# Performance work log

Hardware: AMD Instinct MI355X
Metric: run time of the kernel (lower is better)

The kernel has to match this reference:

```python
import jax, jax.numpy as jnp
import numpy as np

BETA = 0.25


def setup_inputs() -> dict:
    key = jax.random.key(0)
    k1, k2 = jax.random.split(key)
    z_e = jax.random.normal(k1, (32, 256, 32, 32), dtype=jnp.float32)
    embedding = jax.random.normal(k2, (1024, 256), dtype=jnp.float32)
    return {"z_e": z_e, "embedding": embedding}


def reference(z_e, embedding):
    B, D, H, W = z_e.shape  # (32, 256, 32, 32)
    K = embedding.shape[0]
    # flatten to (N, D), N = B*H*W
    z_flat = jnp.transpose(z_e, (0, 2, 3, 1)).reshape(-1, D)
    # squared L2 distances: ||z||^2 + ||e||^2 - 2 z.e^T  -> (N, K)
    dist = (
        jnp.sum(z_flat * z_flat, axis=1, keepdims=True)
        + jnp.sum(embedding * embedding, axis=1)
        - 2.0 * z_flat @ embedding.T
    )
    codes = jnp.argmin(dist, axis=1)  # (N,) int
    # gather codebook vectors, reshape back to (B, D, H, W)
    z_q = embedding[codes].reshape(B, H, W, D).transpose(0, 3, 1, 2)
    # commitment loss (mse over all elements)
    sg = jax.lax.stop_gradient
    commit_loss = (
        jnp.mean((sg(z_q) - z_e) ** 2)
        + BETA * jnp.mean((z_q - sg(z_e)) ** 2)
    )
    # straight-through estimator
    z_q_st = z_e + sg(z_q - z_e)
    return z_q_st, codes.reshape(B, H, W), commit_loss
```

## Files before the change

### kernel.cpp

```cpp
#include <hip/hip_runtime.h>

typedef _Float16 f16;
typedef __attribute__((ext_vector_type(4))) _Float16 f16x4;
typedef __attribute__((ext_vector_type(8))) _Float16 f16x8;
typedef __attribute__((ext_vector_type(4))) float f32x4;

#define D_DIM 256
#define K_CB  1024
#define N_TOT 32768
#define DHW   262144
#define ZQ_N  8388608
#define OUT_CODES 8388608
#define OUT_LOSS  8421376

#define WS_BSP   0
#define WS_EN2   262144
#define WS_CODES 263168
#define WS_CNT   295936
#define WS_LIST  296000
#define WS_PART  300096
#define LIST_CAP 4096
#define EPS_GAP  0.01f

__global__ void vq_prep(const float* __restrict__ emb, float* __restrict__ ws) {
    const int k = blockIdx.x;
    const int t = threadIdx.x;
    const float4 v = *reinterpret_cast<const float4*>(emb + k * D_DIM + t * 4);
    float s = v.x * v.x + v.y * v.y + v.z * v.z + v.w * v.w;
#pragma unroll
    for (int off = 32; off > 0; off >>= 1) s += __shfl_down(s, off);
    if (t == 0) ws[WS_EN2 + k] = -0.5f * s;

    const float a[4] = {v.x, v.y, v.z, v.w};
    f16x4 hv, lv;
#pragma unroll
    for (int i = 0; i < 4; ++i) {
        f16 h = (f16)a[i];
        hv[i] = h;
        lv[i] = (f16)(a[i] - (float)h);
    }
    f16* B = reinterpret_cast<f16*>(ws) + k * 512;
    *reinterpret_cast<f16x4*>(B + t * 4)       = hv;
    *reinterpret_cast<f16x4*>(B + 256 + t * 4) = lv;
    if (k == 0 && t == 0) reinterpret_cast<int*>(ws + WS_CNT)[0] = 0;
}

__global__ __launch_bounds__(256, 2) void vq_gemm(const float* __restrict__ z,
                                                  float* ws,
                                                  float* __restrict__ out) {
    __shared__ __align__(16) char lds[81920];
    f16* Ahi = reinterpret_cast<f16*>(lds);
    f16* Alo = reinterpret_cast<f16*>(lds + 32768);
    f16* Bs  = reinterpret_cast<f16*>(lds + 65536);
    float* comb = reinterpret_cast<float*>(lds + 65536);

    const f16* __restrict__ Bsp = reinterpret_cast<const f16*>(ws);
    const float* __restrict__ en2 = ws + WS_EN2;
    const int tid = threadIdx.x;
    const int lane = tid & 63;
    const int w = tid >> 6, wm = w >> 1, wn = w & 1;
    const int r0 = blockIdx.x * 64;
    const float* __restrict__ zb = z + (r0 >> 10) * DHW + (r0 & 1023);

    {
        const int arow = tid & 63;
        const int adg  = tid >> 6;
#pragma unroll
        for (int p = 0; p < 16; ++p) {
            const int d = adg * 64 + p * 4;
            f16x4 hv, lv;
#pragma unroll
            for (int i = 0; i < 4; ++i) {
                const float x = zb[(d + i) * 1024 + arow];
                const f16 h = (f16)x;
                hv[i] = h;
                lv[i] = (f16)(x - (float)h);
            }
            const int byte = (arow * 512 + d * 2) ^ ((arow & 7) << 4);
            *reinterpret_cast<f16x4*>(reinterpret_cast<char*>(Ahi) + byte) = hv;
            *reinterpret_cast<f16x4*>(reinterpret_cast<char*>(Alo) + byte) = lv;
        }
    }

    float bv[8], sv[8];
    int   bk[8];
#pragma unroll
    for (int i = 0; i < 8; ++i) { bv[i] = -3.0e38f; sv[i] = -3.0e38f; bk[i] = 0; }

    f32x4 acc[2][4];
#pragma unroll
    for (int i = 0; i < 2; ++i)
#pragma unroll
        for (int j = 0; j < 4; ++j) acc[i][j] = f32x4{0.f, 0.f, 0.f, 0.f};

    f16x8 breg[4], bnext[4];
    float e2v[4];
#pragma unroll
    for (int p = 0; p < 4; ++p) {
        const int u = tid + p * 256;
        breg[p] = *reinterpret_cast<const f16x8*>(
            Bsp + (u >> 3) * 512 + (u & 7) * 8);
    }

    for (int q = 0; q < 64; ++q) {
        __syncthreads();
#pragma unroll
        for (int p = 0; p < 4; ++p) {
            const int u = tid + p * 256;
            const int col = u >> 3, k8 = (u & 7) * 8;
            const int byte = (col * 128 + k8 * 2) ^ ((col & 7) << 4);
            *reinterpret_cast<f16x8*>(reinterpret_cast<char*>(Bs) + byte) = breg[p];
        }
        if (q < 63) {
            const int qn = q + 1;
            const int c0n = (qn >> 3) << 7;
            const int kbn = (qn & 7) << 6;
#pragma unroll
            for (int p = 0; p < 4; ++p) {
                const int u = tid + p * 256;
                bnext[p] = *reinterpret_cast<const f16x8*>(
                    Bsp + (c0n + (u >> 3)) * 512 + kbn + (u & 7) * 8);
            }
        }
        if ((q & 7) == 6) {
            const int c0 = (q >> 3) << 7;
#pragma unroll
            for (int jf = 0; jf < 4; ++jf)
                e2v[jf] = en2[c0 + wn * 64 + jf * 16 + (lane & 15)];
        }
        __syncthreads();

        const int kA = (q & 3) << 6;
        const bool ehi = ((q >> 2) & 1) == 0;
#pragma unroll
        for (int s = 0; s < 2; ++s) {
            const int kl = s * 32 + (lane >> 4) * 8;
            f16x8 bf[4];
#pragma unroll
            for (int jf = 0; jf < 4; ++jf) {
                const int cc = wn * 64 + jf * 16 + (lane & 15);
                bf[jf] = *reinterpret_cast<const f16x8*>(
                    reinterpret_cast<const char*>(Bs) +
                    ((cc * 128 + kl * 2) ^ ((cc & 7) << 4)));
            }
            f16x8 ah[2];
#pragma unroll
            for (int i = 0; i < 2; ++i) {
                const int row = wm * 32 + i * 16 + (lane & 15);
                ah[i] = *reinterpret_cast<const f16x8*>(
                    reinterpret_cast<const char*>(Ahi) +
                    ((row * 512 + (kA + kl) * 2) ^ ((row & 7) << 4)));
            }
#pragma unroll
            for (int i = 0; i < 2; ++i)
#pragma unroll
                for (int jf = 0; jf < 4; ++jf)
                    acc[i][jf] = __builtin_amdgcn_mfma_f32_16x16x32_f16(
                        ah[i], bf[jf], acc[i][jf], 0, 0, 0);
            if (ehi) {
                f16x8 al[2];
#pragma unroll
                for (int i = 0; i < 2; ++i) {
                    const int row = wm * 32 + i * 16 + (lane & 15);
                    al[i] = *reinterpret_cast<const f16x8*>(
                        reinterpret_cast<const char*>(Alo) +
                        ((row * 512 + (kA + kl) * 2) ^ ((row & 7) << 4)));
                }
#pragma unroll
                for (int i = 0; i < 2; ++i)
#pragma unroll
                    for (int jf = 0; jf < 4; ++jf)
                        acc[i][jf] = __builtin_amdgcn_mfma_f32_16x16x32_f16(
                            al[i], bf[jf], acc[i][jf], 0, 0, 0);
            }
        }

        if ((q & 7) == 7) {
            const int c0 = (q >> 3) << 7;
#pragma unroll
            for (int jf = 0; jf < 4; ++jf) {
                const int col = c0 + wn * 64 + jf * 16 + (lane & 15);
                const float e2 = e2v[jf];
#pragma unroll
                for (int i = 0; i < 2; ++i)
#pragma unroll
                    for (int r = 0; r < 4; ++r) {
                        const float v = acc[i][jf][r] + e2;
                        const int idx = i * 4 + r;
                        if (v > bv[idx]) { sv[idx] = bv[idx]; bv[idx] = v; bk[idx] = col; }
                        else if (v > sv[idx]) sv[idx] = v;
                    }
            }
#pragma unroll
            for (int i = 0; i < 2; ++i)
#pragma unroll
                for (int j = 0; j < 4; ++j) acc[i][j] = f32x4{0.f, 0.f, 0.f, 0.f};
        }
#pragma unroll
        for (int p = 0; p < 4; ++p) breg[p] = bnext[p];
    }

#pragma unroll
    for (int m = 1; m <= 8; m <<= 1)
#pragma unroll
        for (int idx = 0; idx < 8; ++idx) {
            const float pv = __shfl_xor(bv[idx], m);
            const float ps = __shfl_xor(sv[idx], m);
            const int   pk = __shfl_xor(bk[idx], m);
            if (pv > bv[idx] || (pv == bv[idx] && pk < bk[idx])) {
                sv[idx] = fmaxf(bv[idx], ps);
                bv[idx] = pv; bk[idx] = pk;
            } else {
                sv[idx] = fmaxf(sv[idx], pv);
            }
        }

    __syncthreads();
    if ((lane & 15) == 0) {
#pragma unroll
        for (int idx = 0; idx < 8; ++idx) {
            const int row = wm * 32 + (idx >> 2) * 16 + (lane >> 4) * 4 + (idx & 3);
            comb[(wn * 64 + row) * 3 + 0] = bv[idx];
            comb[(wn * 64 + row) * 3 + 1] = sv[idx];
            comb[(wn * 64 + row) * 3 + 2] = __int_as_float(bk[idx]);
        }
    }
    __syncthreads();
    if (tid < 64) {
        const int row = tid;
        const float v0 = comb[row * 3 + 0], s0 = comb[row * 3 + 1];
        const int   k0 = __float_as_int(comb[row * 3 + 2]);
        const float v1 = comb[(64 + row) * 3 + 0], s1 = comb[(64 + row) * 3 + 1];
        const int   k1 = __float_as_int(comb[(64 + row) * 3 + 2]);
        float bvf, svf; int bkf;
        if (v1 > v0 || (v1 == v0 && k1 < k0)) { bvf = v1; bkf = k1; svf = fmaxf(v0, s1); }
        else                                  { bvf = v0; bkf = k0; svf = fmaxf(s0, v1); }
        const int n = r0 + row;
        reinterpret_cast<int*>(ws + WS_CODES)[n] = bkf;
        out[OUT_CODES + n] = (float)bkf;
        if (bvf - svf < EPS_GAP) {
            const int pos = atomicAdd(reinterpret_cast<int*>(ws + WS_CNT), 1);
            if (pos < LIST_CAP) reinterpret_cast<int*>(ws + WS_LIST)[pos] = n;
        }
    }
}

__global__ __launch_bounds__(256) void vq_rescore(const float* __restrict__ z,
                                                  const float* __restrict__ emb,
                                                  float* ws,
                                                  float* __restrict__ out) {
    __shared__ float zl[256];
    __shared__ float rv[4];
    __shared__ int   rk[4];
    const int cnt0 = reinterpret_cast<const int*>(ws + WS_CNT)[0];
    const int cnt = cnt0 < LIST_CAP ? cnt0 : LIST_CAP;
    const int t = threadIdx.x;
    for (int it = blockIdx.x; it < cnt; it += gridDim.x) {
        const int n = reinterpret_cast<const int*>(ws + WS_LIST)[it];
        const int b = n >> 10, hw = n & 1023;
        __syncthreads();
        zl[t] = z[b * DHW + t * 1024 + hw];
        __syncthreads();
        float bvv = -3.0e38f; int bkk = 0;
#pragma unroll
        for (int j = 0; j < 4; ++j) {
            const int k = t + j * 256;
            const float* e = emb + k * D_DIM;
            float dot = 0.f;
#pragma unroll 8
            for (int d = 0; d < 256; d += 4) {
                const float4 ev = *reinterpret_cast<const float4*>(e + d);
                const float4 zv = *reinterpret_cast<const float4*>(zl + d);
                dot += ev.x * zv.x + ev.y * zv.y + ev.z * zv.z + ev.w * zv.w;
            }
            const float v = dot + ws[WS_EN2 + k];
            if (v > bvv || (v == bvv && k < bkk)) { bvv = v; bkk = k; }
        }
#pragma unroll
        for (int m = 1; m <= 32; m <<= 1) {
            const float pv = __shfl_xor(bvv, m);
            const int   pk = __shfl_xor(bkk, m);
            if (pv > bvv || (pv == bvv && pk < bkk)) { bvv = pv; bkk = pk; }
        }
        if ((t & 63) == 0) { rv[t >> 6] = bvv; rk[t >> 6] = bkk; }
        __syncthreads();
        if (t == 0) {
#pragma unroll
            for (int q = 1; q < 4; ++q)
                if (rv[q] > bvv || (rv[q] == bvv && rk[q] < bkk)) { bvv = rv[q]; bkk = rk[q]; }
            reinterpret_cast<int*>(ws + WS_CODES)[n] = bkk;
            out[OUT_CODES + n] = (float)bkk;
        }
    }
}

__global__ __launch_bounds__(256) void vq_gather(const float* __restrict__ z,
                                                 const float* __restrict__ emb,
                                                 float* ws,
                                                 float* __restrict__ out) {
    __shared__ __align__(16) float el[64][260];
    __shared__ int   cl[64];
    __shared__ float red[4];
    const int tid = threadIdx.x;
    const int n0 = blockIdx.x * 64;
    const int b = n0 >> 10, hw0 = n0 & 1023;
    if (tid < 64) cl[tid] = reinterpret_cast<const int*>(ws + WS_CODES)[n0 + tid];
    __syncthreads();
#pragma unroll
    for (int p = 0; p < 16; ++p) {
        const int u = tid + p * 256;
        const int r = u >> 6, f4 = (u & 63) * 4;
        *reinterpret_cast<float4*>(&el[r][f4]) =
            *reinterpret_cast<const float4*>(emb + cl[r] * D_DIM + f4);
    }
    __syncthreads();
    const int hw4 = (tid & 15) * 4, dg = tid >> 4;
    const float* zp = z + b * DHW + hw0 + hw4;
    float* op = out + b * DHW + hw0 + hw4;
    float ls = 0.f;
#pragma unroll
    for (int dd = 0; dd < 16; ++dd) {
        const int d = dg * 16 + dd;
        float4 q;
        q.x = el[hw4 + 0][d]; q.y = el[hw4 + 1][d];
        q.z = el[hw4 + 2][d]; q.w = el[hw4 + 3][d];
        const float4 zv = *reinterpret_cast<const float4*>(zp + d * 1024);
        *reinterpret_cast<float4*>(op + d * 1024) = q;
        const float dx = q.x - zv.x, dy = q.y - zv.y;
        const float dz = q.z - zv.z, dw = q.w - zv.w;
        ls += dx * dx + dy * dy + dz * dz + dw * dw;
    }
#pragma unroll
    for (int m = 32; m > 0; m >>= 1) ls += __shfl_down(ls, m);
    if ((tid & 63) == 0) red[tid >> 6] = ls;
    __syncthreads();
    if (tid == 0) ws[WS_PART + blockIdx.x] = red[0] + red[1] + red[2] + red[3];
}

__global__ __launch_bounds__(256) void vq_finalize(const float* __restrict__ ws,
                                                   float* __restrict__ out) {
    __shared__ float red[4];
    const int t = threadIdx.x;
    float s = ws[WS_PART + t] + ws[WS_PART + t + 256];
#pragma unroll
    for (int off = 32; off > 0; off >>= 1) s += __shfl_down(s, off);
    if ((t & 63) == 0) red[t >> 6] = s;
    __syncthreads();
    if (t == 0)
        out[OUT_LOSS] = (red[0] + red[1] + red[2] + red[3]) * (1.25f / 8388608.0f);
}

extern "C" void kernel_launch(void* const* d_in, const int* in_sizes, int n_in,
                              void* d_out, int out_size, void* d_ws, size_t ws_size,
                              hipStream_t stream) {
    const float* z   = (const float*)d_in[0];
    const float* emb = (const float*)d_in[1];
    float* out = (float*)d_out;
    float* ws  = (float*)d_ws;

    vq_prep<<<K_CB, 64, 0, stream>>>(emb, ws);
    vq_gemm<<<N_TOT / 64, 256, 0, stream>>>(z, ws, out);
    vq_rescore<<<64, 256, 0, stream>>>(z, emb, ws, out);
    vq_gather<<<ZQ_N / (256 * 64), 256, 0, stream>>>(z, emb, ws, out);
    vq_finalize<<<1, 256, 0, stream>>>(ws, out);
}
```

Before: 204.5 us.

## Drop split-fp16 low term, widen near-tie rescoring, compute loss from best distance

```diff
diff --git a/kernel.cpp b/kernel.cpp
--- a/kernel.cpp
+++ b/kernel.cpp
@@ -14,13 +14,13 @@
 #define OUT_LOSS  8421376
 
 #define WS_BSP   0
-#define WS_EN2   262144
-#define WS_CODES 263168
-#define WS_CNT   295936
-#define WS_LIST  296000
-#define WS_PART  300096
-#define LIST_CAP 4096
-#define EPS_GAP  0.01f
+#define WS_EN2   131072
+#define WS_CODES 132096
+#define WS_CNT   164864
+#define WS_LIST  164928
+#define WS_RLOSS 197696
+#define LIST_CAP 32768
+#define EPS_GAP  0.08f
 
 __global__ void vq_prep(const float* __restrict__ emb, float* __restrict__ ws) {
     const int k = blockIdx.x;
@@ -30,159 +30,130 @@
 #pragma unroll
     for (int off = 32; off > 0; off >>= 1) s += __shfl_down(s, off);
     if (t == 0) ws[WS_EN2 + k] = -0.5f * s;
-
     const float a[4] = {v.x, v.y, v.z, v.w};
-    f16x4 hv, lv;
-#pragma unroll
-    for (int i = 0; i < 4; ++i) {
-        f16 h = (f16)a[i];
-        hv[i] = h;
-        lv[i] = (f16)(a[i] - (float)h);
-    }
-    f16* B = reinterpret_cast<f16*>(ws) + k * 512;
-    *reinterpret_cast<f16x4*>(B + t * 4)       = hv;
-    *reinterpret_cast<f16x4*>(B + 256 + t * 4) = lv;
+    f16x4 hv;
+#pragma unroll
+    for (int i = 0; i < 4; ++i) hv[i] = (f16)a[i];
+    *reinterpret_cast<f16x4*>(reinterpret_cast<f16*>(ws) + k * 256 + t * 4) = hv;
     if (k == 0 && t == 0) reinterpret_cast<int*>(ws + WS_CNT)[0] = 0;
 }
 
 __global__ __launch_bounds__(256, 2) void vq_gemm(const float* __restrict__ z,
                                                   float* ws,
                                                   float* __restrict__ out) {
-    __shared__ __align__(16) char lds[81920];
+    __shared__ __align__(16) char lds[66560];
     f16* Ahi = reinterpret_cast<f16*>(lds);
-    f16* Alo = reinterpret_cast<f16*>(lds + 32768);
-    f16* Bs  = reinterpret_cast<f16*>(lds + 65536);
-    float* comb = reinterpret_cast<float*>(lds + 65536);
+    f16* Bs  = reinterpret_cast<f16*>(lds + 32768);
+    float* rowsum = reinterpret_cast<float*>(lds + 65536);
+    float* comb = reinterpret_cast<float*>(lds + 32768);
 
     const f16* __restrict__ Bsp = reinterpret_cast<const f16*>(ws);
     const float* __restrict__ en2 = ws + WS_EN2;
     const int tid = threadIdx.x;
     const int lane = tid & 63;
-    const int w = tid >> 6, wm = w >> 1, wn = w & 1;
+    const int w = tid >> 6;
     const int r0 = blockIdx.x * 64;
     const float* __restrict__ zb = z + (r0 >> 10) * DHW + (r0 & 1023);
 
     {
         const int arow = tid & 63;
         const int adg  = tid >> 6;
+        float sq = 0.f;
 #pragma unroll
         for (int p = 0; p < 16; ++p) {
             const int d = adg * 64 + p * 4;
-            f16x4 hv, lv;
+            f16x4 hv;
 #pragma unroll
             for (int i = 0; i < 4; ++i) {
                 const float x = zb[(d + i) * 1024 + arow];
-                const f16 h = (f16)x;
-                hv[i] = h;
-                lv[i] = (f16)(x - (float)h);
+                hv[i] = (f16)x;
+                sq += x * x;
             }
             const int byte = (arow * 512 + d * 2) ^ ((arow & 7) << 4);
             *reinterpret_cast<f16x4*>(reinterpret_cast<char*>(Ahi) + byte) = hv;
-            *reinterpret_cast<f16x4*>(reinterpret_cast<char*>(Alo) + byte) = lv;
-        }
-    }
-
-    float bv[8], sv[8];
-    int   bk[8];
-#pragma unroll
-    for (int i = 0; i < 8; ++i) { bv[i] = -3.0e38f; sv[i] = -3.0e38f; bk[i] = 0; }
-
-    f32x4 acc[2][4];
-#pragma unroll
-    for (int i = 0; i < 2; ++i)
+        }
+        rowsum[adg * 64 + arow] = sq;
+    }
+
+    float bv[16], sv[16];
+    int   bk[16];
+#pragma unroll
+    for (int i = 0; i < 16; ++i) { bv[i] = -3.0e38f; sv[i] = -3.0e38f; bk[i] = 0; }
+
+    f32x4 acc[4][4];
+#pragma unroll
+    for (int i = 0; i < 4; ++i)
 #pragma unroll
         for (int j = 0; j < 4; ++j) acc[i][j] = f32x4{0.f, 0.f, 0.f, 0.f};
 
-    f16x8 breg[4], bnext[4];
+    f16x8 breg[8];
+#pragma unroll
+    for (int p = 0; p < 8; ++p) {
+        const int u = tid + p * 256;
+        breg[p] = *reinterpret_cast<const f16x8*>(Bsp + (u >> 3) * 256 + (u & 7) * 8);
+    }
     float e2v[4];
-#pragma unroll
-    for (int p = 0; p < 4; ++p) {
-        const int u = tid + p * 256;
-        breg[p] = *reinterpret_cast<const f16x8*>(
-            Bsp + (u >> 3) * 512 + (u & 7) * 8);
-    }
-
-    for (int q = 0; q < 64; ++q) {
-        __syncthreads();
-#pragma unroll
-        for (int p = 0; p < 4; ++p) {
+
+    for (int q = 0; q < 16; ++q) {
+        __syncthreads();
+#pragma unroll
+        for (int p = 0; p < 8; ++p) {
             const int u = tid + p * 256;
             const int col = u >> 3, k8 = (u & 7) * 8;
             const int byte = (col * 128 + k8 * 2) ^ ((col & 7) << 4);
             *reinterpret_cast<f16x8*>(reinterpret_cast<char*>(Bs) + byte) = breg[p];
         }
-        if (q < 63) {
+        if ((q & 3) == 2) {
+            const int c0 = (q >> 2) * 256;
+#pragma unroll
+            for (int jf = 0; jf < 4; ++jf)
+                e2v[jf] = en2[c0 + w * 64 + jf * 16 + (lane & 15)];
+        }
+        __syncthreads();
+        if (q < 15) {
             const int qn = q + 1;
-            const int c0n = (qn >> 3) << 7;
-            const int kbn = (qn & 7) << 6;
-#pragma unroll
-            for (int p = 0; p < 4; ++p) {
+            const int c0n = (qn >> 2) * 256, kbn = (qn & 3) * 64;
+#pragma unroll
+            for (int p = 0; p < 8; ++p) {
                 const int u = tid + p * 256;
-                bnext[p] = *reinterpret_cast<const f16x8*>(
-                    Bsp + (c0n + (u >> 3)) * 512 + kbn + (u & 7) * 8);
-            }
-        }
-        if ((q & 7) == 6) {
-            const int c0 = (q >> 3) << 7;
-#pragma unroll
-            for (int jf = 0; jf < 4; ++jf)
-                e2v[jf] = en2[c0 + wn * 64 + jf * 16 + (lane & 15)];
-        }
-        __syncthreads();
-
-        const int kA = (q & 3) << 6;
-        const bool ehi = ((q >> 2) & 1) == 0;
+                breg[p] = *reinterpret_cast<const f16x8*>(
+                    Bsp + (c0n + (u >> 3)) * 256 + kbn + (u & 7) * 8);
+            }
+        }
+        const int kA = (q & 3) * 64;
 #pragma unroll
         for (int s = 0; s < 2; ++s) {
             const int kl = s * 32 + (lane >> 4) * 8;
-            f16x8 bf[4];
+            f16x8 bf[4], af[4];
 #pragma unroll
             for (int jf = 0; jf < 4; ++jf) {
-                const int cc = wn * 64 + jf * 16 + (lane & 15);
+                const int col = w * 64 + jf * 16 + (lane & 15);
                 bf[jf] = *reinterpret_cast<const f16x8*>(
                     reinterpret_cast<const char*>(Bs) +
-                    ((cc * 128 + kl * 2) ^ ((cc & 7) << 4)));
-            }
-            f16x8 ah[2];
-#pragma unroll
-            for (int i = 0; i < 2; ++i) {
-                const int row = wm * 32 + i * 16 + (lane & 15);
-                ah[i] = *reinterpret_cast<const f16x8*>(
+                    ((col * 128 + kl * 2) ^ ((col & 7) << 4)));
+            }
+#pragma unroll
+            for (int i = 0; i < 4; ++i) {
+                const int row = i * 16 + (lane & 15);
+                af[i] = *reinterpret_cast<const f16x8*>(
                     reinterpret_cast<const char*>(Ahi) +
                     ((row * 512 + (kA + kl) * 2) ^ ((row & 7) << 4)));
             }
 #pragma unroll
-            for (int i = 0; i < 2; ++i)
+            for (int i = 0; i < 4; ++i)
 #pragma unroll
                 for (int jf = 0; jf < 4; ++jf)
                     acc[i][jf] = __builtin_amdgcn_mfma_f32_16x16x32_f16(
-                        ah[i], bf[jf], acc[i][jf], 0, 0, 0);
-            if (ehi) {
-                f16x8 al[2];
-#pragma unroll
-                for (int i = 0; i < 2; ++i) {
-                    const int row = wm * 32 + i * 16 + (lane & 15);
-                    al[i] = *reinterpret_cast<const f16x8*>(
-                        reinterpret_cast<const char*>(Alo) +
-                        ((row * 512 + (kA + kl) * 2) ^ ((row & 7) << 4)));
-                }
-#pragma unroll
-                for (int i = 0; i < 2; ++i)
-#pragma unroll
-                    for (int jf = 0; jf < 4; ++jf)
-                        acc[i][jf] = __builtin_amdgcn_mfma_f32_16x16x32_f16(
-                            al[i], bf[jf], acc[i][jf], 0, 0, 0);
-            }
-        }
-
-        if ((q & 7) == 7) {
-            const int c0 = (q >> 3) << 7;
+                        af[i], bf[jf], acc[i][jf], 0, 0, 0);
+        }
+        if ((q & 3) == 3) {
+            const int c0 = (q >> 2) * 256;
 #pragma unroll
             for (int jf = 0; jf < 4; ++jf) {
-                const int col = c0 + wn * 64 + jf * 16 + (lane & 15);
+                const int col = c0 + w * 64 + jf * 16 + (lane & 15);
                 const float e2 = e2v[jf];
 #pragma unroll
-                for (int i = 0; i < 2; ++i)
+                for (int i = 0; i < 4; ++i)
 #pragma unroll
                     for (int r = 0; r < 4; ++r) {
                         const float v = acc[i][jf][r] + e2;
@@ -192,18 +163,16 @@
                     }
             }
 #pragma unroll
-            for (int i = 0; i < 2; ++i)
+            for (int i = 0; i < 4; ++i)
 #pragma unroll
                 for (int j = 0; j < 4; ++j) acc[i][j] = f32x4{0.f, 0.f, 0.f, 0.f};
         }
-#pragma unroll
-        for (int p = 0; p < 4; ++p) breg[p] = bnext[p];
     }
 
 #pragma unroll
     for (int m = 1; m <= 8; m <<= 1)
 #pragma unroll
-        for (int idx = 0; idx < 8; ++idx) {
+        for (int idx = 0; idx < 16; ++idx) {
             const float pv = __shfl_xor(bv[idx], m);
             const float ps = __shfl_xor(sv[idx], m);
             const int   pk = __shfl_xor(bk[idx], m);
@@ -218,26 +187,32 @@
     __syncthreads();
     if ((lane & 15) == 0) {
 #pragma unroll
-        for (int idx = 0; idx < 8; ++idx) {
-            const int row = wm * 32 + (idx >> 2) * 16 + (lane >> 4) * 4 + (idx & 3);
-            comb[(wn * 64 + row) * 3 + 0] = bv[idx];
-            comb[(wn * 64 + row) * 3 + 1] = sv[idx];
-            comb[(wn * 64 + row) * 3 + 2] = __int_as_float(bk[idx]);
+        for (int idx = 0; idx < 16; ++idx) {
+            const int row = (idx >> 2) * 16 + (lane >> 4) * 4 + (idx & 3);
+            comb[(w * 64 + row) * 3 + 0] = bv[idx];
+            comb[(w * 64 + row) * 3 + 1] = sv[idx];
+            comb[(w * 64 + row) * 3 + 2] = __int_as_float(bk[idx]);
         }
     }
     __syncthreads();
     if (tid < 64) {
         const int row = tid;
-        const float v0 = comb[row * 3 + 0], s0 = comb[row * 3 + 1];
-        const int   k0 = __float_as_int(comb[row * 3 + 2]);
-        const float v1 = comb[(64 + row) * 3 + 0], s1 = comb[(64 + row) * 3 + 1];
-        const int   k1 = __float_as_int(comb[(64 + row) * 3 + 2]);
-        float bvf, svf; int bkf;
-        if (v1 > v0 || (v1 == v0 && k1 < k0)) { bvf = v1; bkf = k1; svf = fmaxf(v0, s1); }
-        else                                  { bvf = v0; bkf = k0; svf = fmaxf(s0, v1); }
+        float bvf = comb[row * 3 + 0], svf = comb[row * 3 + 1];
+        int   bkf = __float_as_int(comb[row * 3 + 2]);
+#pragma unroll
+        for (int q2 = 1; q2 < 4; ++q2) {
+            const float v = comb[(q2 * 64 + row) * 3 + 0];
+            const float s2 = comb[(q2 * 64 + row) * 3 + 1];
+            const int   k2 = __float_as_int(comb[(q2 * 64 + row) * 3 + 2]);
+            if (v > bvf) { svf = fmaxf(bvf, s2); bvf = v; bkf = k2; }
+            else         { svf = fmaxf(svf, v); }
+        }
         const int n = r0 + row;
         reinterpret_cast<int*>(ws + WS_CODES)[n] = bkf;
         out[OUT_CODES + n] = (float)bkf;
+        const float znorm = rowsum[row] + rowsum[64 + row] +
+                            rowsum[128 + row] + rowsum[192 + row];
+        ws[WS_RLOSS + n] = znorm - 2.f * bvf;
         if (bvf - svf < EPS_GAP) {
             const int pos = atomicAdd(reinterpret_cast<int*>(ws + WS_CNT), 1);
             if (pos < LIST_CAP) reinterpret_cast<int*>(ws + WS_LIST)[pos] = n;
@@ -250,6 +225,7 @@
                                                   float* ws,
                                                   float* __restrict__ out) {
     __shared__ float zl[256];
+    __shared__ float zred[4];
     __shared__ float rv[4];
     __shared__ int   rk[4];
     const int cnt0 = reinterpret_cast<const int*>(ws + WS_CNT)[0];
@@ -259,7 +235,12 @@
         const int n = reinterpret_cast<const int*>(ws + WS_LIST)[it];
         const int b = n >> 10, hw = n & 1023;
         __syncthreads();
-        zl[t] = z[b * DHW + t * 1024 + hw];
+        const float x = z[b * DHW + t * 1024 + hw];
+        zl[t] = x;
+        float zs = x * x;
+#pragma unroll
+        for (int off = 32; off > 0; off >>= 1) zs += __shfl_down(zs, off);
+        if ((t & 63) == 0) zred[t >> 6] = zs;
         __syncthreads();
         float bvv = -3.0e38f; int bkk = 0;
 #pragma unroll
@@ -290,17 +271,17 @@
                 if (rv[q] > bvv || (rv[q] == bvv && rk[q] < bkk)) { bvv = rv[q]; bkk = rk[q]; }
             reinterpret_cast<int*>(ws + WS_CODES)[n] = bkk;
             out[OUT_CODES + n] = (float)bkk;
-        }
-    }
-}
-
-__global__ __launch_bounds__(256) void vq_gather(const float* __restrict__ z,
-                                                 const float* __restrict__ emb,
+            const float znorm = zred[0] + zred[1] + zred[2] + zred[3];
+            ws[WS_RLOSS + n] = znorm - 2.f * bvv;
+        }
+    }
+}
+
+__global__ __launch_bounds__(256) void vq_gather(const float* __restrict__ emb,
                                                  float* ws,
                                                  float* __restrict__ out) {
     __shared__ __align__(16) float el[64][260];
-    __shared__ int   cl[64];
-    __shared__ float red[4];
+    __shared__ int cl[64];
     const int tid = threadIdx.x;
     const int n0 = blockIdx.x * 64;
     const int b = n0 >> 10, hw0 = n0 & 1023;
@@ -315,33 +296,28 @@
     }
     __syncthreads();
     const int hw4 = (tid & 15) * 4, dg = tid >> 4;
-    const float* zp = z + b * DHW + hw0 + hw4;
     float* op = out + b * DHW + hw0 + hw4;
-    float ls = 0.f;
 #pragma unroll
     for (int dd = 0; dd < 16; ++dd) {
         const int d = dg * 16 + dd;
         float4 q;
         q.x = el[hw4 + 0][d]; q.y = el[hw4 + 1][d];
         q.z = el[hw4 + 2][d]; q.w = el[hw4 + 3][d];
-        const float4 zv = *reinterpret_cast<const float4*>(zp + d * 1024);
         *reinterpret_cast<float4*>(op + d * 1024) = q;
-        const float dx = q.x - zv.x, dy = q.y - zv.y;
-        const float dz = q.z - zv.z, dw = q.w - zv.w;
-        ls += dx * dx + dy * dy + dz * dz + dw * dw;
-    }
-#pragma unroll
-    for (int m = 32; m > 0; m >>= 1) ls += __shfl_down(ls, m);
-    if ((tid & 63) == 0) red[tid >> 6] = ls;
-    __syncthreads();
-    if (tid == 0) ws[WS_PART + blockIdx.x] = red[0] + red[1] + red[2] + red[3];
+    }
 }
 
 __global__ __launch_bounds__(256) void vq_finalize(const float* __restrict__ ws,
                                                    float* __restrict__ out) {
     __shared__ float red[4];
     const int t = threadIdx.x;
-    float s = ws[WS_PART + t] + ws[WS_PART + t + 256];
+    const float4* rl = reinterpret_cast<const float4*>(ws + WS_RLOSS);
+    float s = 0.f;
+#pragma unroll
+    for (int i = 0; i < 32; ++i) {
+        const float4 v = rl[t + i * 256];
+        s += v.x + v.y + v.z + v.w;
+    }
 #pragma unroll
     for (int off = 32; off > 0; off >>= 1) s += __shfl_down(s, off);
     if ((t & 63) == 0) red[t >> 6] = s;
@@ -360,7 +336,7 @@
 
     vq_prep<<<K_CB, 64, 0, stream>>>(emb, ws);
     vq_gemm<<<N_TOT / 64, 256, 0, stream>>>(z, ws, out);
-    vq_rescore<<<64, 256, 0, stream>>>(z, emb, ws, out);
-    vq_gather<<<ZQ_N / (256 * 64), 256, 0, stream>>>(z, emb, ws, out);
+    vq_rescore<<<256, 256, 0, stream>>>(z, emb, ws, out);
+    vq_gather<<<ZQ_N / (256 * 64), 256, 0, stream>>>(emb, ws, out);
     vq_finalize<<<1, 256, 0, stream>>>(ws, out);
 }
```

Result: slower. 218.1 us (+6.7%).
